# Kernel optimization log

Measured on AMD Instinct MI355X. Metric: run time of the kernel, lower is better.

## Reference

```python
import jax, jax.numpy as jnp
import numpy as np

N_QUBITS = 10


def _apply_1q(state, U, wire, n):
    # state: (B, 2**n) complex; apply 2x2 U on `wire` (wire 0 = most significant bit)
    B = state.shape[0]
    left = 2 ** wire
    right = 2 ** (n - wire - 1)
    s = state.reshape(B, left, 2, right)
    s = jnp.einsum('ij,bljr->blir', U, s)
    return s.reshape(B, 2 ** n)


def _cnot(state, c, t, n):
    # CNOT with control wire c, target wire t
    B = state.shape[0]
    s = state.reshape((B,) + (2,) * n)
    ci, ti = c + 1, t + 1
    flipped = jnp.flip(s, axis=ti)
    zero = jnp.take(s, 0, axis=ci)      # control=0 slice unchanged
    one = jnp.take(flipped, 1, axis=ci)  # control=1 slice with target flipped
    s = jnp.stack([zero, one], axis=ci)
    return s.reshape(B, 2 ** n)


def _rot_matrix(phi, theta, omega):
    # PennyLane Rot(phi, theta, omega) = RZ(omega) @ RY(theta) @ RZ(phi)
    c = jnp.cos(theta / 2).astype(jnp.complex64)
    s = jnp.sin(theta / 2).astype(jnp.complex64)
    ep = jnp.exp(-0.5j * (phi + omega).astype(jnp.complex64))  # e^{-i(phi+omega)/2}
    em = jnp.exp(0.5j * (phi - omega).astype(jnp.complex64))   # e^{ i(phi-omega)/2}
    row0 = jnp.stack([ep * c, -em * s])
    row1 = jnp.stack([jnp.conj(em) * s, jnp.conj(ep) * c])
    return jnp.stack([row0, row1])  # (2, 2)


def setup_inputs() -> dict:
    key = jax.random.key(0)
    k1, k2 = jax.random.split(key)
    B, dim = 8192, 2 ** N_QUBITS
    patch = jax.random.normal(k1, (B, dim), dtype=jnp.float32)
    patch = patch / jnp.linalg.norm(patch, axis=1, keepdims=True)  # L2-normalized amplitudes
    weights = 0.01 * jax.random.normal(k2, (N_QUBITS, 3), dtype=jnp.float32)
    return {"patch_batch": patch, "weights": weights}


def reference(patch_batch, weights):
    n = weights.shape[0]
    state = patch_batch.astype(jnp.complex64)  # amplitude embedding
    for w in range(n):
        U = _rot_matrix(weights[w, 0], weights[w, 1], weights[w, 2])
        state = _apply_1q(state, U, w, n)
    for w in range(n - 1):
        state = _cnot(state, w, w + 1, n)
    state = _cnot(state, n - 1, 0, n)
    # expectation values of X, Y, Z on wire 0
    s2 = state.reshape(-1, 2, 2 ** (n - 1))
    a0, a1 = s2[:, 0], s2[:, 1]
    z = jnp.sum(jnp.conj(a0) * a1, axis=1)
    ex = 2.0 * jnp.real(z)
    ey = 2.0 * jnp.imag(z)
    ez = jnp.sum(jnp.abs(a0) ** 2 - jnp.abs(a1) ** 2, axis=1)
    out = jnp.stack([ex, ey, ez], axis=1)  # (B, 3)
    return jnp.nan_to_num(out, nan=0.0, posinf=1.0, neginf=-1.0)
```

## Files before the change

### kernel.cpp

```cpp
#include <hip/hip_runtime.h>


typedef float v2f __attribute__((ext_vector_type(2)));

__device__ __forceinline__ v2f psplat(float k) { v2f r; r.x = k; r.y = k; return r; }
__device__ __forceinline__ v2f pfma(float k, v2f a, v2f b) {
    return __builtin_elementwise_fma(psplat(k), a, b);
}

template <int CTRL>
__device__ __forceinline__ float dppf(float x) {
    return __int_as_float(__builtin_amdgcn_update_dpp(
        __float_as_int(x), __float_as_int(x), CTRL, 0xF, 0xF, true));
}

template <int MASK>
__device__ __forceinline__ float lxor(float x) {
    if constexpr (MASK == 1)  return dppf<0xB1>(x);
    else if constexpr (MASK == 2)  return dppf<0x4E>(x);
    else if constexpr (MASK == 4)  return dppf<0x141>(dppf<0x1B>(x));
    else if constexpr (MASK == 8)  return dppf<0x128>(x);
    else if constexpr (MASK == 16)
        return __int_as_float(__builtin_amdgcn_ds_swizzle(__float_as_int(x), 0x401F));
    else return __shfl_xor(x, MASK, 64);
}

__global__ void qk_setup(const float* __restrict__ w, float* __restrict__ ws) {
    int t = threadIdx.x;
    float a = 0.f;
    for (int wq = 0; wq < 10; wq++)
        if ((t >> (9 - wq)) & 1) a += w[3 * wq];
    ws[2 * t]     = cosf(a);
    ws[2 * t + 1] = sinf(a);
    if (t < 10) {
        float th = w[3 * t + 1];
        ws[2048 + 2 * t]     = cosf(0.5f * th);
        ws[2048 + 2 * t + 1] = sinf(0.5f * th);
    }
    if (t < 4) {
        float d = (1.f - 2.f * ((t >> 1) & 1)) * w[2] + (1.f - 2.f * (t & 1)) * w[5];
        ws[2068 + 2 * t]     = cosf(d);
        ws[2068 + 2 * t + 1] = sinf(d);
    }
}

__device__ __forceinline__ void rgate(v2f (&amp)[16], int bit, float c, float s) {
#pragma unroll
    for (int s0 = 0; s0 < 16; s0++) {
        if (s0 & bit) continue;
        int s1 = s0 | bit;
        v2f a0 = amp[s0], a1 = amp[s1];
        amp[s0] = pfma(-s, a1, psplat(c) * a0);
        amp[s1] = pfma( s, a0, psplat(c) * a1);
    }
}

template <int MASK>
__device__ __forceinline__ void xgate(v2f (&amp)[16], float c, float ss) {
#pragma unroll
    for (int r = 0; r < 16; r++) {
        v2f p;
        p.x = lxor<MASK>(amp[r].x);
        p.y = lxor<MASK>(amp[r].y);
        amp[r] = pfma(ss, p, psplat(c) * amp[r]);
    }
}

__global__ __launch_bounds__(256) void qk_sim(const float* __restrict__ x,
                                              const float* __restrict__ ws,
                                              float* __restrict__ out,
                                              int nstates) {
    int wave = (int)((blockIdx.x * blockDim.x + threadIdx.x) >> 6);
    int lane = threadIdx.x & 63;

    const float* CS = ws + 2048;
    const float* T4 = ws + 2068;

    const float4* rowx = (const float4*)(x + (size_t)wave * 1024);
    const float4* Pt   = (const float4*)ws;
    v2f amp[16];
#pragma unroll
    for (int h = 0; h < 4; h++) {
        float4 v  = rowx[h * 64 + lane];
        float4 p0 = Pt[h * 128 + lane * 2];
        float4 p1 = Pt[h * 128 + lane * 2 + 1];
        v2f q0; q0.x = p0.x; q0.y = p0.y;
        v2f q1; q1.x = p0.z; q1.y = p0.w;
        v2f q2; q2.x = p1.x; q2.y = p1.y;
        v2f q3; q3.x = p1.z; q3.y = p1.w;
        amp[h * 4 + 0] = psplat(v.x) * q0;
        amp[h * 4 + 1] = psplat(v.y) * q1;
        amp[h * 4 + 2] = psplat(v.z) * q2;
        amp[h * 4 + 3] = psplat(v.w) * q3;
    }

    rgate(amp, 1, CS[2 * 9], CS[2 * 9 + 1]);
    rgate(amp, 2, CS[2 * 8], CS[2 * 8 + 1]);
    rgate(amp, 4, CS[2 * 1], CS[2 * 1 + 1]);
    rgate(amp, 8, CS[2 * 0], CS[2 * 0 + 1]);

    {
        float s7 = CS[2 * 7 + 1], s6 = CS[2 * 6 + 1], s5 = CS[2 * 5 + 1];
        float s4 = CS[2 * 4 + 1], s3 = CS[2 * 3 + 1], s2 = CS[2 * 2 + 1];
        xgate<1> (amp, CS[2 * 7], (lane & 1)  ? s7 : -s7);
        xgate<2> (amp, CS[2 * 6], (lane & 2)  ? s6 : -s6);
        xgate<4> (amp, CS[2 * 5], (lane & 4)  ? s5 : -s5);
        xgate<8> (amp, CS[2 * 4], (lane & 8)  ? s4 : -s4);
        xgate<16>(amp, CS[2 * 3], (lane & 16) ? s3 : -s3);
        xgate<32>(amp, CS[2 * 2], (lane & 32) ? s2 : -s2);
    }

    float ex2 = 0.f, ey2 = 0.f;
    v2f ezv = psplat(0.f);
#pragma unroll
    for (int h = 0; h < 2; h++) {
        float cD = T4[2 * h], sD = T4[2 * h + 1];
#pragma unroll
        for (int q = 0; q < 4; q++) {
            int s  = h * 4 + q;
            int sp = s ^ 12;
            v2f m = amp[s], p = amp[sp];
            float cr = m.x * p.x + m.y * p.y;
            float ci = m.x * p.y - m.y * p.x;
            ex2 += cD * cr - sD * ci;
            float t = cD * ci + sD * cr;
            if ((h ^ (__popc(q) & 1)) & 1) ey2 -= t; else ey2 += t;
        }
    }
#pragma unroll
    for (int s = 0; s < 16; s++) {
        v2f n = amp[s] * amp[s];
        if ((((s >> 2) & 1) ^ (__popc(s & 3) & 1)) & 1) ezv -= n; else ezv += n;
    }
    float psgn = (__popc(lane) & 1) ? -1.f : 1.f;
    v2f exy;
    exy.x = 2.f * ex2;
    exy.y = 2.f * psgn * ey2;
    float ez = psgn * (ezv.x + ezv.y);

#define RED(M) { v2f o; o.x = lxor<M>(exy.x); o.y = lxor<M>(exy.y); exy += o; \
                 ez += lxor<M>(ez); }
    RED(1) RED(2) RED(4) RED(8) RED(16) RED(32)
#undef RED

    if (lane == 0) {
        float* o = out + 3 * (size_t)wave;
        o[0] = exy.x; o[1] = exy.y; o[2] = ez;
    }
}

extern "C" void kernel_launch(void* const* d_in, const int* in_sizes, int n_in,
                              void* d_out, int out_size, void* d_ws, size_t ws_size,
                              hipStream_t stream) {
    const float* patch   = (const float*)d_in[0];
    const float* weights = (const float*)d_in[1];
    float* out = (float*)d_out;
    float* ws  = (float*)d_ws;

    int nstates = in_sizes[0] / 1024;

    qk_setup<<<1, 1024, 0, stream>>>(weights, ws);

    int nblocks = nstates / 4;
    qk_sim<<<nblocks, 256, 0, stream>>>(patch, ws, out, nstates);
}
```

Before: 82.63 us.

## Fuse setup kernel into sim kernel, compute phases and gate trig per wave

```diff
diff --git a/kernel.cpp b/kernel.cpp
--- a/kernel.cpp
+++ b/kernel.cpp
@@ -25,24 +25,7 @@
     else return __shfl_xor(x, MASK, 64);
 }
 
-__global__ void qk_setup(const float* __restrict__ w, float* __restrict__ ws) {
-    int t = threadIdx.x;
-    float a = 0.f;
-    for (int wq = 0; wq < 10; wq++)
-        if ((t >> (9 - wq)) & 1) a += w[3 * wq];
-    ws[2 * t]     = cosf(a);
-    ws[2 * t + 1] = sinf(a);
-    if (t < 10) {
-        float th = w[3 * t + 1];
-        ws[2048 + 2 * t]     = cosf(0.5f * th);
-        ws[2048 + 2 * t + 1] = sinf(0.5f * th);
-    }
-    if (t < 4) {
-        float d = (1.f - 2.f * ((t >> 1) & 1)) * w[2] + (1.f - 2.f * (t & 1)) * w[5];
-        ws[2068 + 2 * t]     = cosf(d);
-        ws[2068 + 2 * t + 1] = sinf(d);
-    }
-}
+#define RLF(v, l) __int_as_float(__builtin_amdgcn_readlane(__float_as_int(v), (l)))
 
 __device__ __forceinline__ void rgate(v2f (&amp)[16], int bit, float c, float s) {
 #pragma unroll
@@ -67,54 +50,75 @@
 }
 
 __global__ __launch_bounds__(256) void qk_sim(const float* __restrict__ x,
-                                              const float* __restrict__ ws,
+                                              const float* __restrict__ w,
                                               float* __restrict__ out,
                                               int nstates) {
     int wave = (int)((blockIdx.x * blockDim.x + threadIdx.x) >> 6);
     int lane = threadIdx.x & 63;
 
-    const float* CS = ws + 2048;
-    const float* T4 = ws + 2068;
+    int wi = (lane < 10) ? lane : 0;
+    float thh = 0.5f * w[3 * wi + 1];
+    float vc = __cosf(thh), vs = __sinf(thh);
+    float c0 = RLF(vc, 0), s0 = RLF(vs, 0);
+    float c1 = RLF(vc, 1), s1 = RLF(vs, 1);
+    float c2 = RLF(vc, 2), s2 = RLF(vs, 2);
+    float c3 = RLF(vc, 3), s3 = RLF(vs, 3);
+    float c4 = RLF(vc, 4), s4 = RLF(vs, 4);
+    float c5 = RLF(vc, 5), s5 = RLF(vs, 5);
+    float c6 = RLF(vc, 6), s6 = RLF(vs, 6);
+    float c7 = RLF(vc, 7), s7 = RLF(vs, 7);
+    float c8 = RLF(vc, 8), s8 = RLF(vs, 8);
+    float c9 = RLF(vc, 9), s9 = RLF(vs, 9);
+
+    float om0 = w[2], om1 = w[5];
+    float cD0 = __cosf(om0 + om1), sD0 = __sinf(om0 + om1);
+    float cD1 = __cosf(om0 - om1), sD1 = __sinf(om0 - om1);
+
+    float aL = 0.f;
+    if (lane & 1)  aL += w[21];
+    if (lane & 2)  aL += w[18];
+    if (lane & 4)  aL += w[15];
+    if (lane & 8)  aL += w[12];
+    if (lane & 16) aL += w[9];
+    if (lane & 32) aL += w[6];
+    float pH = w[0], pHb = w[3];
+    float pQ = w[24], pQb = w[27];
+    float aH[4] = {0.f, pHb, pH, pH + pHb};
+    float aQ[4] = {0.f, pQb, pQ, pQ + pQb};
 
     const float4* rowx = (const float4*)(x + (size_t)wave * 1024);
-    const float4* Pt   = (const float4*)ws;
     v2f amp[16];
 #pragma unroll
     for (int h = 0; h < 4; h++) {
-        float4 v  = rowx[h * 64 + lane];
-        float4 p0 = Pt[h * 128 + lane * 2];
-        float4 p1 = Pt[h * 128 + lane * 2 + 1];
-        v2f q0; q0.x = p0.x; q0.y = p0.y;
-        v2f q1; q1.x = p0.z; q1.y = p0.w;
-        v2f q2; q2.x = p1.x; q2.y = p1.y;
-        v2f q3; q3.x = p1.z; q3.y = p1.w;
-        amp[h * 4 + 0] = psplat(v.x) * q0;
-        amp[h * 4 + 1] = psplat(v.y) * q1;
-        amp[h * 4 + 2] = psplat(v.z) * q2;
-        amp[h * 4 + 3] = psplat(v.w) * q3;
+        float4 v = rowx[h * 64 + lane];
+        float base = aL + aH[h];
+        float xv[4] = {v.x, v.y, v.z, v.w};
+#pragma unroll
+        for (int q = 0; q < 4; q++) {
+            float a = base + aQ[q];
+            v2f e; e.x = __cosf(a); e.y = __sinf(a);
+            amp[h * 4 + q] = psplat(xv[q]) * e;
+        }
     }
 
-    rgate(amp, 1, CS[2 * 9], CS[2 * 9 + 1]);
-    rgate(amp, 2, CS[2 * 8], CS[2 * 8 + 1]);
-    rgate(amp, 4, CS[2 * 1], CS[2 * 1 + 1]);
-    rgate(amp, 8, CS[2 * 0], CS[2 * 0 + 1]);
+    rgate(amp, 1, c9, s9);
+    rgate(amp, 2, c8, s8);
+    rgate(amp, 4, c1, s1);
+    rgate(amp, 8, c0, s0);
 
-    {
-        float s7 = CS[2 * 7 + 1], s6 = CS[2 * 6 + 1], s5 = CS[2 * 5 + 1];
-        float s4 = CS[2 * 4 + 1], s3 = CS[2 * 3 + 1], s2 = CS[2 * 2 + 1];
-        xgate<1> (amp, CS[2 * 7], (lane & 1)  ? s7 : -s7);
-        xgate<2> (amp, CS[2 * 6], (lane & 2)  ? s6 : -s6);
-        xgate<4> (amp, CS[2 * 5], (lane & 4)  ? s5 : -s5);
-        xgate<8> (amp, CS[2 * 4], (lane & 8)  ? s4 : -s4);
-        xgate<16>(amp, CS[2 * 3], (lane & 16) ? s3 : -s3);
-        xgate<32>(amp, CS[2 * 2], (lane & 32) ? s2 : -s2);
-    }
+    xgate<1> (amp, c7, (lane & 1)  ? s7 : -s7);
+    xgate<2> (amp, c6, (lane & 2)  ? s6 : -s6);
+    xgate<4> (amp, c5, (lane & 4)  ? s5 : -s5);
+    xgate<8> (amp, c4, (lane & 8)  ? s4 : -s4);
+    xgate<16>(amp, c3, (lane & 16) ? s3 : -s3);
+    xgate<32>(amp, c2, (lane & 32) ? s2 : -s2);
 
     float ex2 = 0.f, ey2 = 0.f;
     v2f ezv = psplat(0.f);
 #pragma unroll
     for (int h = 0; h < 2; h++) {
-        float cD = T4[2 * h], sD = T4[2 * h + 1];
+        float cD = h ? cD1 : cD0;
+        float sD = h ? sD1 : sD0;
 #pragma unroll
         for (int q = 0; q < 4; q++) {
             int s  = h * 4 + q;
@@ -155,12 +159,9 @@
     const float* patch   = (const float*)d_in[0];
     const float* weights = (const float*)d_in[1];
     float* out = (float*)d_out;
-    float* ws  = (float*)d_ws;
 
     int nstates = in_sizes[0] / 1024;
 
-    qk_setup<<<1, 1024, 0, stream>>>(weights, ws);
-
     int nblocks = nstates / 4;
-    qk_sim<<<nblocks, 256, 0, stream>>>(patch, ws, out, nstates);
+    qk_sim<<<nblocks, 256, 0, stream>>>(patch, weights, out, nstates);
 }
```

Measured after the change: 82.54 us. About the same (-0.1%).
